# Performance work log

Hardware: AMD Instinct MI355X
Metric: run time of the kernel (lower is better)

The kernel has to match this reference:

```python
import jax, jax.numpy as jnp
import numpy as np

NEG_SLOPE = 0.2


def gat_conv(x, src, dst, W, a_src, a_dst, bias, heads, out_ch, concat, num_nodes):
    # x: [N, F_in]; W: [F_in, heads*out_ch]; a_src/a_dst: [heads, out_ch]
    h = (x @ W).reshape(num_nodes, heads, out_ch)                 # [N,H,C]
    alpha_s = jnp.sum(h * a_src[None], axis=-1)                   # [N,H]
    alpha_d = jnp.sum(h * a_dst[None], axis=-1)                   # [N,H]
    e = jax.nn.leaky_relu(alpha_s[src] + alpha_d[dst], NEG_SLOPE)  # [E,H]
    # numerically-stable segment softmax over incoming edges of each dst node
    e_max = jax.ops.segment_max(e, dst, num_segments=num_nodes)   # [N,H]
    e_exp = jnp.exp(e - e_max[dst])                               # [E,H]
    denom = jax.ops.segment_sum(e_exp, dst, num_segments=num_nodes)
    alpha = e_exp / (denom[dst] + 1e-16)                          # [E,H]
    msg = h[src] * alpha[:, :, None]                              # [E,H,C]
    out = jax.ops.segment_sum(msg, dst, num_segments=num_nodes)   # [N,H,C]
    if concat:
        out = out.reshape(num_nodes, heads * out_ch)
    else:
        out = out.mean(axis=1)
    return out + bias


def setup_inputs() -> dict:
    key = jax.random.key(0)
    ks = jax.random.split(key, 16)
    N, E = 100000, 1600000
    F_in, Hid, Out, Heads = 128, 64, 16, 1
    s = lambda k, shp, fan: jax.random.normal(k, shp, dtype=jnp.float32) * (1.0 / np.sqrt(fan))
    return {
        "x": jax.random.normal(ks[0], (N, F_in), dtype=jnp.float32),
        "edge_index": jax.random.randint(ks[1], (2, E), 0, N, dtype=jnp.int32),
        "W1": s(ks[2], (F_in, Heads * Hid), F_in),
        "a_src1": s(ks[3], (Heads, Hid), Hid),
        "a_dst1": s(ks[4], (Heads, Hid), Hid),
        "b1": jnp.zeros((Heads * Hid,), jnp.float32),
        "W2": s(ks[5], (Heads * Hid, Out), Heads * Hid),
        "a_src2": s(ks[6], (1, Out), Out),
        "a_dst2": s(ks[7], (1, Out), Out),
        "b2": jnp.zeros((Out,), jnp.float32),
        "lin1_W": s(ks[8], (Out, Hid), Out),
        "lin1_b": jnp.zeros((Hid,), jnp.float32),
        "lin2_W": s(ks[9], (Hid, Out), Hid),
        "lin2_b": jnp.zeros((Out,), jnp.float32),
    }


def reference(x, edge_index, W1, a_src1, a_dst1, b1, W2, a_src2, a_dst2, b2,
              lin1_W, lin1_b, lin2_W, lin2_b):
    N = x.shape[0]
    # PyG GATConv adds self-loops by default
    loop = jnp.arange(N, dtype=edge_index.dtype)
    src = jnp.concatenate([edge_index[0], loop])
    dst = jnp.concatenate([edge_index[1], loop])

    h = gat_conv(x, src, dst, W1, a_src1, a_dst1, b1,
                 heads=1, out_ch=64, concat=True, num_nodes=N)
    h = jax.nn.relu(h)
    h = gat_conv(h, src, dst, W2, a_src2, a_dst2, b2,
                 heads=1, out_ch=16, concat=False, num_nodes=N)
    h = jax.nn.relu(h @ lin1_W + lin1_b)
    h = h @ lin2_W + lin2_b
    return jax.nn.softmax(h, axis=-1)
```

## Files before the change

kernel.cpp:

```cpp
#include <hip/hip_runtime.h>

#define FIN 128
#define HID 64
#define OUTC 16
#define R1 16
#define BSH 8
#define MAXNB 512

__global__ __launch_bounds__(256) void k1_gemm1(
    const float* __restrict__ x, const float* __restrict__ W1,
    const float* __restrict__ a_src, const float* __restrict__ a_dst,
    float* __restrict__ h1, float* __restrict__ as1, float* __restrict__ ad1, int N)
{
    __shared__ float Wlds[FIN * HID];
    __shared__ float xlds[R1 * FIN];
    int tid = threadIdx.x;
    const float4* W4 = (const float4*)W1;
    float4* Wl4 = (float4*)Wlds;
    #pragma unroll
    for (int i = tid; i < FIN * HID / 4; i += 256) Wl4[i] = W4[i];
    int row0 = blockIdx.x * R1;
    const float4* x4 = (const float4*)(x + (size_t)row0 * FIN);
    float4* xl4 = (float4*)xlds;
    for (int i = tid; i < R1 * FIN / 4; i += 256) {
        int r = row0 + (i >> 5);
        xl4[i] = (r < N) ? x4[i] : make_float4(0.f, 0.f, 0.f, 0.f);
    }
    __syncthreads();
    int col = tid & 63;
    int wv  = tid >> 6;
    float acc[4] = {0.f, 0.f, 0.f, 0.f};
    #pragma unroll 4
    for (int k = 0; k < FIN; ++k) {
        float w = Wlds[k * HID + col];
        #pragma unroll
        for (int r = 0; r < 4; ++r)
            acc[r] += xlds[(wv * 4 + r) * FIN + k] * w;
    }
    #pragma unroll
    for (int r = 0; r < 4; ++r) {
        int row = row0 + wv * 4 + r;
        if (row < N) {
            h1[(size_t)row * HID + col] = acc[r];
            float vs = acc[r] * a_src[col];
            float vd = acc[r] * a_dst[col];
            for (int off = 32; off > 0; off >>= 1) {
                vs += __shfl_down(vs, off);
                vd += __shfl_down(vd, off);
            }
            if (col == 0) { as1[row] = vs; ad1[row] = vd; }
        }
    }
}

__global__ __launch_bounds__(256) void kp_cnt(
    const int* __restrict__ ei, int* __restrict__ bcnt, int E, int N)
{
    __shared__ int h[MAXNB];
    int tot = E + N;
    for (int i = threadIdx.x; i < MAXNB; i += 256) h[i] = 0;
    __syncthreads();
    int t0 = blockIdx.x * 4096;
    int n = min(4096, tot - t0);
    for (int i = threadIdx.x; i < n; i += 256) {
        int e = t0 + i;
        int d = (e < E) ? ei[E + e] : (e - E);
        atomicAdd(&h[d >> BSH], 1);
    }
    __syncthreads();
    int nb = (N + 255) >> BSH;
    for (int b = threadIdx.x; b < nb; b += 256)
        if (h[b]) atomicAdd(&bcnt[b], h[b]);
}

__global__ __launch_bounds__(512) void kp_scan(
    const int* __restrict__ bcnt, int* __restrict__ bstartE, int* __restrict__ bcur, int N)
{
    __shared__ int sA[512], sB[512];
    int nb = (N + 255) >> BSH;
    int tid = threadIdx.x;
    int c = (tid < nb) ? bcnt[tid] : 0;
    sA[tid] = c;
    __syncthreads();
    int* src = sA; int* dst = sB;
    for (int off = 1; off < 512; off <<= 1) {
        int v = src[tid];
        if (tid >= off) v += src[tid - off];
        dst[tid] = v;
        __syncthreads();
        int* t = src; src = dst; dst = t;
    }
    int incl = src[tid];
    int excl = incl - c;
    if (tid < nb) {
        bstartE[tid] = excl;
        bcur[tid] = excl;
        if (tid == nb - 1) bstartE[nb] = incl;
    }
}

__global__ __launch_bounds__(256) void kp_part(
    const int* __restrict__ ei, int* __restrict__ bcur, uint2* __restrict__ pairs,
    int E, int N)
{
    __shared__ int sL[4096], dL[4096];
    __shared__ int cnt[MAXNB], base[MAXNB], wcur[MAXNB];
    int tot = E + N;
    for (int i = threadIdx.x; i < MAXNB; i += 256) { cnt[i] = 0; wcur[i] = 0; }
    int t0 = blockIdx.x * 4096;
    int n = min(4096, tot - t0);
    for (int i = threadIdx.x; i < n; i += 256) {
        int e = t0 + i; int s, d;
        if (e < E) { s = ei[e]; d = ei[E + e]; } else { s = d = e - E; }
        sL[i] = s; dL[i] = d;
    }
    __syncthreads();
    for (int i = threadIdx.x; i < n; i += 256) atomicAdd(&cnt[dL[i] >> BSH], 1);
    __syncthreads();
    int nb = (N + 255) >> BSH;
    for (int b = threadIdx.x; b < nb; b += 256) {
        int c = cnt[b];
        if (c) base[b] = atomicAdd(&bcur[b], c);
    }
    __syncthreads();
    for (int i = threadIdx.x; i < n; i += 256) {
        int b = dL[i] >> BSH;
        int r = atomicAdd(&wcur[b], 1);
        pairs[base[b] + r] = make_uint2((unsigned)sL[i], (unsigned)dL[i]);
    }
}

__global__ __launch_bounds__(256) void kc_fine(
    const uint2* __restrict__ pairs, const int* __restrict__ bstartE,
    int* __restrict__ rowstart, int* __restrict__ counts, int* __restrict__ ssrc, int N)
{
    __shared__ int ncnt[256], nsA[256], nsB[256], nst[256];
    int blk = blockIdx.x, tid = threadIdx.x;
    int node0 = blk << BSH;
    int e0 = bstartE[blk], e1 = bstartE[blk + 1];
    ncnt[tid] = 0;
    __syncthreads();
    for (int i = e0 + tid; i < e1; i += 256)
        atomicAdd(&ncnt[pairs[i].y - node0], 1);
    __syncthreads();
    int c = ncnt[tid];
    nsA[tid] = c;
    __syncthreads();
    int* s = nsA; int* d = nsB;
    for (int off = 1; off < 256; off <<= 1) {
        int v = s[tid];
        if (tid >= off) v += s[tid - off];
        d[tid] = v;
        __syncthreads();
        int* t = s; s = d; d = t;
    }
    int excl = s[tid] - c;
    int node = node0 + tid;
    if (node < N) { rowstart[node] = e0 + excl; counts[node] = c; }
    __syncthreads();
    nst[tid] = excl;
    ncnt[tid] = 0;
    __syncthreads();
    for (int i = e0 + tid; i < e1; i += 256) {
        uint2 p = pairs[i];
        int dl = (int)p.y - node0;
        int r = atomicAdd(&ncnt[dl], 1);
        ssrc[e0 + nst[dl] + r] = (int)p.x;
    }
}

__global__ __launch_bounds__(256) void k_gat1(
    const int* __restrict__ rowstart, const int* __restrict__ counts,
    const int* __restrict__ ssrc,
    const float* __restrict__ as, const float* __restrict__ ad,
    const float* __restrict__ h, float* __restrict__ outp, int N)
{
    int wid = (blockIdx.x * 256 + threadIdx.x) >> 6;
    int lane = threadIdx.x & 63;
    if (wid >= N) return;
    int start = rowstart[wid];
    int deg   = counts[wid];
    float adv = ad[wid];
    float acc = 0.f, den = 0.f;
    int j = 0;
    for (; j + 4 <= deg; j += 4) {
        int s0 = ssrc[start + j + 0];
        int s1 = ssrc[start + j + 1];
        int s2 = ssrc[start + j + 2];
        int s3 = ssrc[start + j + 3];
        float a0 = as[s0], a1 = as[s1], a2 = as[s2], a3 = as[s3];
        float h0 = h[(size_t)s0 * HID + lane];
        float h1v = h[(size_t)s1 * HID + lane];
        float h2v = h[(size_t)s2 * HID + lane];
        float h3v = h[(size_t)s3 * HID + lane];
        float v0 = a0 + adv; v0 = (v0 > 0.f) ? v0 : 0.2f * v0; float w0 = __expf(v0);
        float v1 = a1 + adv; v1 = (v1 > 0.f) ? v1 : 0.2f * v1; float w1 = __expf(v1);
        float v2 = a2 + adv; v2 = (v2 > 0.f) ? v2 : 0.2f * v2; float w2 = __expf(v2);
        float v3 = a3 + adv; v3 = (v3 > 0.f) ? v3 : 0.2f * v3; float w3 = __expf(v3);
        den += (w0 + w1) + (w2 + w3);
        acc += w0 * h0;
        acc += w1 * h1v;
        acc += w2 * h2v;
        acc += w3 * h3v;
    }
    for (; j < deg; ++j) {
        int s = ssrc[start + j];
        float v = as[s] + adv;
        v = (v > 0.f) ? v : 0.2f * v;
        float w = __expf(v);
        den += w;
        acc += w * h[(size_t)s * HID + lane];
    }
    outp[(size_t)wid * HID + lane] = acc / (den + 1e-16f);
}

__global__ __launch_bounds__(256) void k4_gemm2(
    const float* __restrict__ out1, const float* __restrict__ b1,
    const float* __restrict__ W2, const float* __restrict__ a_src, const float* __restrict__ a_dst,
    float* __restrict__ h2, float* __restrict__ as2, float* __restrict__ ad2, int N)
{
    __shared__ float Wlds[HID * OUTC];
    __shared__ float rlds[16 * HID];
    int tid = threadIdx.x;
    for (int i = tid; i < HID * OUTC; i += 256) Wlds[i] = W2[i];
    int row0 = blockIdx.x * 16;
    for (int i = tid; i < 16 * HID; i += 256) {
        int r = row0 + (i >> 6);
        float v = (r < N) ? out1[(size_t)r * HID + (i & 63)] : 0.f;
        v += b1[i & 63];
        rlds[i] = fmaxf(v, 0.f);
    }
    __syncthreads();
    int col = tid & 15;
    int rl  = tid >> 4;
    int row = row0 + rl;
    float acc = 0.f;
    #pragma unroll 8
    for (int k = 0; k < HID; ++k)
        acc += rlds[rl * HID + k] * Wlds[k * OUTC + col];
    if (row < N) {
        h2[(size_t)row * OUTC + col] = acc;
        float vs = acc * a_src[col];
        float vd = acc * a_dst[col];
        for (int off = 8; off > 0; off >>= 1) {
            vs += __shfl_down(vs, off, 16);
            vd += __shfl_down(vd, off, 16);
        }
        if (col == 0) { as2[row] = vs; ad2[row] = vd; }
    }
}

__global__ __launch_bounds__(256) void k_gat2(
    const int* __restrict__ rowstart, const int* __restrict__ counts,
    const int* __restrict__ ssrc,
    const float* __restrict__ as, const float* __restrict__ ad,
    const float* __restrict__ h, float* __restrict__ outp, int N)
{
    int wid = (blockIdx.x * 256 + threadIdx.x) >> 6;
    int lane = threadIdx.x & 63;
    int c  = lane & 15;
    int eo = lane >> 4;
    if (wid >= N) return;
    int start = rowstart[wid];
    int deg   = counts[wid];
    float adv = ad[wid];
    float acc = 0.f, den = 0.f;
    int j = eo;
    for (; j + 4 < deg; j += 8) {
        int s0 = ssrc[start + j];
        int s1 = ssrc[start + j + 4];
        float a0 = as[s0], a1 = as[s1];
        float h0 = h[(size_t)s0 * OUTC + c];
        float h1v = h[(size_t)s1 * OUTC + c];
        float v0 = a0 + adv; v0 = (v0 > 0.f) ? v0 : 0.2f * v0; float w0 = __expf(v0);
        float v1 = a1 + adv; v1 = (v1 > 0.f) ? v1 : 0.2f * v1; float w1 = __expf(v1);
        den += w0 + w1;
        acc += w0 * h0;
        acc += w1 * h1v;
    }
    if (j < deg) {
        int s = ssrc[start + j];
        float v = as[s] + adv;
        v = (v > 0.f) ? v : 0.2f * v;
        float w = __expf(v);
        den += w;
        acc += w * h[(size_t)s * OUTC + c];
    }
    acc += __shfl_xor(acc, 16); den += __shfl_xor(den, 16);
    acc += __shfl_xor(acc, 32); den += __shfl_xor(den, 32);
    if (eo == 0) outp[(size_t)wid * OUTC + c] = acc / (den + 1e-16f);
}

__global__ __launch_bounds__(256) void k7_mlp(
    const float* __restrict__ out2, const float* __restrict__ b2,
    const float* __restrict__ lin1W, const float* __restrict__ lin1b,
    const float* __restrict__ lin2W, const float* __restrict__ lin2b,
    float* __restrict__ out, int N)
{
    __shared__ float W1l[OUTC * HID];
    __shared__ float W2l[HID * OUTC];
    __shared__ float b1l[HID], bb2[OUTC], b2l[OUTC];
    int tid = threadIdx.x;
    for (int i = tid; i < OUTC * HID; i += 256) { W1l[i] = lin1W[i]; W2l[i] = lin2W[i]; }
    if (tid < HID) b1l[tid] = lin1b[tid];
    if (tid < OUTC) { bb2[tid] = b2[tid]; b2l[tid] = lin2b[tid]; }
    __syncthreads();
    int n = blockIdx.x * 256 + tid;
    if (n >= N) return;

    float o[OUTC];
    const float4* o4 = (const float4*)(out2 + (size_t)n * OUTC);
    #pragma unroll
    for (int i = 0; i < 4; ++i) {
        float4 v = o4[i];
        o[4*i+0] = v.x + bb2[4*i+0];
        o[4*i+1] = v.y + bb2[4*i+1];
        o[4*i+2] = v.z + bb2[4*i+2];
        o[4*i+3] = v.w + bb2[4*i+3];
    }
    float u[OUTC];
    #pragma unroll
    for (int c = 0; c < OUTC; ++c) u[c] = b2l[c];
    for (int j = 0; j < HID; ++j) {
        float t = b1l[j];
        #pragma unroll
        for (int i = 0; i < OUTC; ++i) t += o[i] * W1l[i * HID + j];
        t = fmaxf(t, 0.f);
        #pragma unroll
        for (int c = 0; c < OUTC; ++c) u[c] += t * W2l[j * OUTC + c];
    }
    float m = u[0];
    #pragma unroll
    for (int c = 1; c < OUTC; ++c) m = fmaxf(m, u[c]);
    float sum = 0.f;
    #pragma unroll
    for (int c = 0; c < OUTC; ++c) { u[c] = __expf(u[c] - m); sum += u[c]; }
    float inv = 1.f / sum;
    float4* dst4 = (float4*)(out + (size_t)n * OUTC);
    #pragma unroll
    for (int i = 0; i < 4; ++i) {
        float4 v;
        v.x = u[4*i+0] * inv; v.y = u[4*i+1] * inv;
        v.z = u[4*i+2] * inv; v.w = u[4*i+3] * inv;
        dst4[i] = v;
    }
}

extern "C" void kernel_launch(void* const* d_in, const int* in_sizes, int n_in,
                              void* d_out, int out_size, void* d_ws, size_t ws_size,
                              hipStream_t stream)
{
    const float* x      = (const float*)d_in[0];
    const int*   ei     = (const int*)  d_in[1];
    const float* W1     = (const float*)d_in[2];
    const float* a_src1 = (const float*)d_in[3];
    const float* a_dst1 = (const float*)d_in[4];
    const float* b1     = (const float*)d_in[5];
    const float* W2     = (const float*)d_in[6];
    const float* a_src2 = (const float*)d_in[7];
    const float* a_dst2 = (const float*)d_in[8];
    const float* b2     = (const float*)d_in[9];
    const float* lin1W  = (const float*)d_in[10];
    const float* lin1b  = (const float*)d_in[11];
    const float* lin2W  = (const float*)d_in[12];
    const float* lin2b  = (const float*)d_in[13];
    float* out = (float*)d_out;

    int N = in_sizes[0] / FIN;
    int E = in_sizes[1] / 2;
    int tot = E + N;
    int nb = (N + 255) >> BSH;
    int ntile = (tot + 4095) / 4096;

    float* ws = (float*)d_ws;
    size_t off = 0;
    float* h1    = ws + off; off += (size_t)N * HID;
    float* out1  = ws + off; off += (size_t)N * HID;
    float* as1   = ws + off; off += N;
    float* ad1   = ws + off; off += N;
    float* h2    = ws + off; off += (size_t)N * OUTC;
    float* out2  = ws + off; off += (size_t)N * OUTC;
    float* as2   = ws + off; off += N;
    float* ad2   = ws + off; off += N;
    int* rowstart = (int*)(ws + off); off += N;
    int* counts   = (int*)(ws + off); off += N;
    int* ssrc     = (int*)(ws + off); off += tot;
    int* bcnt     = (int*)(ws + off); off += MAXNB;
    int* bstartE  = (int*)(ws + off); off += MAXNB + 1;
    int* bcur     = (int*)(ws + off); off += MAXNB;
    uint2* pairs  = (uint2*)out1;

    hipMemsetAsync(bcnt, 0, (size_t)nb * sizeof(int), stream);

    kp_cnt <<<ntile, 256, 0, stream>>>(ei, bcnt, E, N);
    kp_scan<<<1, 512, 0, stream>>>(bcnt, bstartE, bcur, N);
    kp_part<<<ntile, 256, 0, stream>>>(ei, bcur, pairs, E, N);
    kc_fine<<<nb, 256, 0, stream>>>(pairs, bstartE, rowstart, counts, ssrc, N);

    k1_gemm1<<<(N + R1 - 1) / R1, 256, 0, stream>>>(x, W1, a_src1, a_dst1, h1, as1, ad1, N);
    k_gat1  <<<(N + 3) / 4, 256, 0, stream>>>(rowstart, counts, ssrc, as1, ad1, h1, out1, N);

    k4_gemm2<<<(N + 15) / 16, 256, 0, stream>>>(out1, b1, W2, a_src2, a_dst2, h2, as2, ad2, N);
    k_gat2  <<<(N + 3) / 4, 256, 0, stream>>>(rowstart, counts, ssrc, as2, ad2, h2, out2, N);

    k7_mlp<<<(N + 255) / 256, 256, 0, stream>>>(out2, b2, lin1W, lin1b, lin2W, lin2b, out, N);
}
```

Measured before the change: 384.4 us.

## Precompute normalized edge attention weights in a separate pass; pack CSR build pairs

```diff
diff --git a/kernel.cpp b/kernel.cpp
--- a/kernel.cpp
+++ b/kernel.cpp
@@ -6,6 +6,11 @@
 #define R1 16
 #define BSH 8
 #define MAXNB 512
+
+__device__ __forceinline__ float lrelu_exp(float v) {
+    v = (v > 0.f) ? v : 0.2f * v;
+    return __expf(v);
+}
 
 __global__ __launch_bounds__(256) void k1_gemm1(
     const float* __restrict__ x, const float* __restrict__ W1,
@@ -30,12 +35,21 @@
     int col = tid & 63;
     int wv  = tid >> 6;
     float acc[4] = {0.f, 0.f, 0.f, 0.f};
+    const float4* xr0 = (const float4*)&xlds[(wv * 4 + 0) * FIN];
+    const float4* xr1 = (const float4*)&xlds[(wv * 4 + 1) * FIN];
+    const float4* xr2 = (const float4*)&xlds[(wv * 4 + 2) * FIN];
+    const float4* xr3 = (const float4*)&xlds[(wv * 4 + 3) * FIN];
     #pragma unroll 4
-    for (int k = 0; k < FIN; ++k) {
-        float w = Wlds[k * HID + col];
-        #pragma unroll
-        for (int r = 0; r < 4; ++r)
-            acc[r] += xlds[(wv * 4 + r) * FIN + k] * w;
+    for (int k4 = 0; k4 < FIN / 4; ++k4) {
+        float w0 = Wlds[(4 * k4 + 0) * HID + col];
+        float w1 = Wlds[(4 * k4 + 1) * HID + col];
+        float w2 = Wlds[(4 * k4 + 2) * HID + col];
+        float w3 = Wlds[(4 * k4 + 3) * HID + col];
+        float4 xv;
+        xv = xr0[k4]; acc[0] += xv.x * w0 + xv.y * w1 + xv.z * w2 + xv.w * w3;
+        xv = xr1[k4]; acc[1] += xv.x * w0 + xv.y * w1 + xv.z * w2 + xv.w * w3;
+        xv = xr2[k4]; acc[2] += xv.x * w0 + xv.y * w1 + xv.z * w2 + xv.w * w3;
+        xv = xr3[k4]; acc[3] += xv.x * w0 + xv.y * w1 + xv.z * w2 + xv.w * w3;
     }
     #pragma unroll
     for (int r = 0; r < 4; ++r) {
@@ -100,10 +114,11 @@
 }
 
 __global__ __launch_bounds__(256) void kp_part(
-    const int* __restrict__ ei, int* __restrict__ bcur, uint2* __restrict__ pairs,
+    const int* __restrict__ ei, int* __restrict__ bcur, unsigned* __restrict__ pairs,
     int E, int N)
 {
-    __shared__ int sL[4096], dL[4096];
+    __shared__ unsigned pk[4096];
+    __shared__ int bL[4096];
     __shared__ int cnt[MAXNB], base[MAXNB], wcur[MAXNB];
     int tot = E + N;
     for (int i = threadIdx.x; i < MAXNB; i += 256) { cnt[i] = 0; wcur[i] = 0; }
@@ -112,10 +127,11 @@
     for (int i = threadIdx.x; i < n; i += 256) {
         int e = t0 + i; int s, d;
         if (e < E) { s = ei[e]; d = ei[E + e]; } else { s = d = e - E; }
-        sL[i] = s; dL[i] = d;
-    }
-    __syncthreads();
-    for (int i = threadIdx.x; i < n; i += 256) atomicAdd(&cnt[dL[i] >> BSH], 1);
+        pk[i] = (unsigned)s | ((unsigned)(d & 255) << 24);
+        bL[i] = d >> BSH;
+    }
+    __syncthreads();
+    for (int i = threadIdx.x; i < n; i += 256) atomicAdd(&cnt[bL[i]], 1);
     __syncthreads();
     int nb = (N + 255) >> BSH;
     for (int b = threadIdx.x; b < nb; b += 256) {
@@ -124,14 +140,14 @@
     }
     __syncthreads();
     for (int i = threadIdx.x; i < n; i += 256) {
-        int b = dL[i] >> BSH;
+        int b = bL[i];
         int r = atomicAdd(&wcur[b], 1);
-        pairs[base[b] + r] = make_uint2((unsigned)sL[i], (unsigned)dL[i]);
+        pairs[base[b] + r] = pk[i];
     }
 }
 
 __global__ __launch_bounds__(256) void kc_fine(
-    const uint2* __restrict__ pairs, const int* __restrict__ bstartE,
+    const unsigned* __restrict__ pairs, const int* __restrict__ bstartE,
     int* __restrict__ rowstart, int* __restrict__ counts, int* __restrict__ ssrc, int N)
 {
     __shared__ int ncnt[256], nsA[256], nsB[256], nst[256];
@@ -141,7 +157,7 @@
     ncnt[tid] = 0;
     __syncthreads();
     for (int i = e0 + tid; i < e1; i += 256)
-        atomicAdd(&ncnt[pairs[i].y - node0], 1);
+        atomicAdd(&ncnt[pairs[i] >> 24], 1);
     __syncthreads();
     int c = ncnt[tid];
     nsA[tid] = c;
@@ -162,56 +178,104 @@
     ncnt[tid] = 0;
     __syncthreads();
     for (int i = e0 + tid; i < e1; i += 256) {
-        uint2 p = pairs[i];
-        int dl = (int)p.y - node0;
+        unsigned p = pairs[i];
+        int dl = (int)(p >> 24);
         int r = atomicAdd(&ncnt[dl], 1);
-        ssrc[e0 + nst[dl] + r] = (int)p.x;
-    }
-}
-
-__global__ __launch_bounds__(256) void k_gat1(
+        ssrc[e0 + nst[dl] + r] = (int)(p & 0xFFFFFFu);
+    }
+}
+
+__global__ __launch_bounds__(256) void k_wnorm(
     const int* __restrict__ rowstart, const int* __restrict__ counts,
-    const int* __restrict__ ssrc,
-    const float* __restrict__ as, const float* __restrict__ ad,
-    const float* __restrict__ h, float* __restrict__ outp, int N)
-{
-    int wid = (blockIdx.x * 256 + threadIdx.x) >> 6;
-    int lane = threadIdx.x & 63;
-    if (wid >= N) return;
-    int start = rowstart[wid];
-    int deg   = counts[wid];
-    float adv = ad[wid];
-    float acc = 0.f, den = 0.f;
+    const int* __restrict__ ssrc, const float* __restrict__ as, const float* __restrict__ ad,
+    float* __restrict__ alpha, int N)
+{
+    int n = blockIdx.x * 256 + threadIdx.x;
+    if (n >= N) return;
+    int start = rowstart[n];
+    int deg   = counts[n];
+    float adv = ad[n];
+    float den = 0.f;
     int j = 0;
     for (; j + 4 <= deg; j += 4) {
         int s0 = ssrc[start + j + 0];
         int s1 = ssrc[start + j + 1];
         int s2 = ssrc[start + j + 2];
         int s3 = ssrc[start + j + 3];
-        float a0 = as[s0], a1 = as[s1], a2 = as[s2], a3 = as[s3];
+        float w0 = lrelu_exp(as[s0] + adv);
+        float w1 = lrelu_exp(as[s1] + adv);
+        float w2 = lrelu_exp(as[s2] + adv);
+        float w3 = lrelu_exp(as[s3] + adv);
+        alpha[start + j + 0] = w0;
+        alpha[start + j + 1] = w1;
+        alpha[start + j + 2] = w2;
+        alpha[start + j + 3] = w3;
+        den += (w0 + w1) + (w2 + w3);
+    }
+    for (; j < deg; ++j) {
+        int s = ssrc[start + j];
+        float w = lrelu_exp(as[s] + adv);
+        alpha[start + j] = w;
+        den += w;
+    }
+    float inv = 1.f / (den + 1e-16f);
+    j = 0;
+    for (; j + 4 <= deg; j += 4) {
+        alpha[start + j + 0] *= inv;
+        alpha[start + j + 1] *= inv;
+        alpha[start + j + 2] *= inv;
+        alpha[start + j + 3] *= inv;
+    }
+    for (; j < deg; ++j) alpha[start + j] *= inv;
+}
+
+__global__ __launch_bounds__(256) void k_gat1(
+    const int* __restrict__ rowstart, const int* __restrict__ counts,
+    const int* __restrict__ ssrc, const float* __restrict__ alpha,
+    const float* __restrict__ h, float* __restrict__ outp, int N)
+{
+    int wid = (blockIdx.x * 256 + threadIdx.x) >> 6;
+    int lane = threadIdx.x & 63;
+    if (wid >= N) return;
+    int start = rowstart[wid];
+    int deg   = counts[wid];
+    float acc = 0.f;
+    int j = 0;
+    for (; j + 8 <= deg; j += 8) {
+        int s0 = ssrc[start + j + 0];
+        int s1 = ssrc[start + j + 1];
+        int s2 = ssrc[start + j + 2];
+        int s3 = ssrc[start + j + 3];
+        int s4 = ssrc[start + j + 4];
+        int s5 = ssrc[start + j + 5];
+        int s6 = ssrc[start + j + 6];
+        int s7 = ssrc[start + j + 7];
+        float a0 = alpha[start + j + 0];
+        float a1 = alpha[start + j + 1];
+        float a2 = alpha[start + j + 2];
+        float a3 = alpha[start + j + 3];
+        float a4 = alpha[start + j + 4];
+        float a5 = alpha[start + j + 5];
+        float a6 = alpha[start + j + 6];
+        float a7 = alpha[start + j + 7];
         float h0 = h[(size_t)s0 * HID + lane];
         float h1v = h[(size_t)s1 * HID + lane];
         float h2v = h[(size_t)s2 * HID + lane];
         float h3v = h[(size_t)s3 * HID + lane];
-        float v0 = a0 + adv; v0 = (v0 > 0.f) ? v0 : 0.2f * v0; float w0 = __expf(v0);
-        float v1 = a1 + adv; v1 = (v1 > 0.f) ? v1 : 0.2f * v1; float w1 = __expf(v1);
-        float v2 = a2 + adv; v2 = (v2 > 0.f) ? v2 : 0.2f * v2; float w2 = __expf(v2);
-        float v3 = a3 + adv; v3 = (v3 > 0.f) ? v3 : 0.2f * v3; float w3 = __expf(v3);
-        den += (w0 + w1) + (w2 + w3);
-        acc += w0 * h0;
-        acc += w1 * h1v;
-        acc += w2 * h2v;
-        acc += w3 * h3v;
+        float h4 = h[(size_t)s4 * HID + lane];
+        float h5 = h[(size_t)s5 * HID + lane];
+        float h6 = h[(size_t)s6 * HID + lane];
+        float h7 = h[(size_t)s7 * HID + lane];
+        acc += a0 * h0;  acc += a1 * h1v;
+        acc += a2 * h2v; acc += a3 * h3v;
+        acc += a4 * h4;  acc += a5 * h5;
+        acc += a6 * h6;  acc += a7 * h7;
     }
     for (; j < deg; ++j) {
         int s = ssrc[start + j];
-        float v = as[s] + adv;
-        v = (v > 0.f) ? v : 0.2f * v;
-        float w = __expf(v);
-        den += w;
-        acc += w * h[(size_t)s * HID + lane];
-    }
-    outp[(size_t)wid * HID + lane] = acc / (den + 1e-16f);
+        acc += alpha[start + j] * h[(size_t)s * HID + lane];
+    }
+    outp[(size_t)wid * HID + lane] = acc;
 }
 
 __global__ __launch_bounds__(256) void k4_gemm2(
@@ -252,8 +316,7 @@
 
 __global__ __launch_bounds__(256) void k_gat2(
     const int* __restrict__ rowstart, const int* __restrict__ counts,
-    const int* __restrict__ ssrc,
-    const float* __restrict__ as, const float* __restrict__ ad,
+    const int* __restrict__ ssrc, const float* __restrict__ alpha,
     const float* __restrict__ h, float* __restrict__ outp, int N)
 {
     int wid = (blockIdx.x * 256 + threadIdx.x) >> 6;
@@ -263,32 +326,25 @@
     if (wid >= N) return;
     int start = rowstart[wid];
     int deg   = counts[wid];
-    float adv = ad[wid];
-    float acc = 0.f, den = 0.f;
+    float acc = 0.f;
     int j = eo;
     for (; j + 4 < deg; j += 8) {
         int s0 = ssrc[start + j];
         int s1 = ssrc[start + j + 4];
-        float a0 = as[s0], a1 = as[s1];
+        float a0 = alpha[start + j];
+        float a1 = alpha[start + j + 4];
         float h0 = h[(size_t)s0 * OUTC + c];
         float h1v = h[(size_t)s1 * OUTC + c];
-        float v0 = a0 + adv; v0 = (v0 > 0.f) ? v0 : 0.2f * v0; float w0 = __expf(v0);
-        float v1 = a1 + adv; v1 = (v1 > 0.f) ? v1 : 0.2f * v1; float w1 = __expf(v1);
-        den += w0 + w1;
-        acc += w0 * h0;
-        acc += w1 * h1v;
+        acc += a0 * h0;
+        acc += a1 * h1v;
     }
     if (j < deg) {
         int s = ssrc[start + j];
-        float v = as[s] + adv;
-        v = (v > 0.f) ? v : 0.2f * v;
-        float w = __expf(v);
-        den += w;
-        acc += w * h[(size_t)s * OUTC + c];
-    }
-    acc += __shfl_xor(acc, 16); den += __shfl_xor(den, 16);
-    acc += __shfl_xor(acc, 32); den += __shfl_xor(den, 32);
-    if (eo == 0) outp[(size_t)wid * OUTC + c] = acc / (den + 1e-16f);
+        acc += alpha[start + j] * h[(size_t)s * OUTC + c];
+    }
+    acc += __shfl_xor(acc, 16);
+    acc += __shfl_xor(acc, 32);
+    if (eo == 0) outp[(size_t)wid * OUTC + c] = acc;
 }
 
 __global__ __launch_bounds__(256) void k7_mlp(
@@ -382,13 +438,14 @@
     float* out2  = ws + off; off += (size_t)N * OUTC;
     float* as2   = ws + off; off += N;
     float* ad2   = ws + off; off += N;
+    float* alpha = ws + off; off += tot;
     int* rowstart = (int*)(ws + off); off += N;
     int* counts   = (int*)(ws + off); off += N;
     int* ssrc     = (int*)(ws + off); off += tot;
     int* bcnt     = (int*)(ws + off); off += MAXNB;
     int* bstartE  = (int*)(ws + off); off += MAXNB + 1;
     int* bcur     = (int*)(ws + off); off += MAXNB;
-    uint2* pairs  = (uint2*)out1;
+    unsigned* pairs = (unsigned*)out1;
 
     hipMemsetAsync(bcnt, 0, (size_t)nb * sizeof(int), stream);
 
@@ -398,10 +455,12 @@
     kc_fine<<<nb, 256, 0, stream>>>(pairs, bstartE, rowstart, counts, ssrc, N);
 
     k1_gemm1<<<(N + R1 - 1) / R1, 256, 0, stream>>>(x, W1, a_src1, a_dst1, h1, as1, ad1, N);
-    k_gat1  <<<(N + 3) / 4, 256, 0, stream>>>(rowstart, counts, ssrc, as1, ad1, h1, out1, N);
+    k_wnorm <<<(N + 255) / 256, 256, 0, stream>>>(rowstart, counts, ssrc, as1, ad1, alpha, N);
+    k_gat1  <<<(N + 3) / 4, 256, 0, stream>>>(rowstart, counts, ssrc, alpha, h1, out1, N);
 
     k4_gemm2<<<(N + 15) / 16, 256, 0, stream>>>(out1, b1, W2, a_src2, a_dst2, h2, as2, ad2, N);
-    k_gat2  <<<(N + 3) / 4, 256, 0, stream>>>(rowstart, counts, ssrc, as2, ad2, h2, out2, N);
+    k_wnorm <<<(N + 255) / 256, 256, 0, stream>>>(rowstart, counts, ssrc, as2, ad2, alpha, N);
+    k_gat2  <<<(N + 3) / 4, 256, 0, stream>>>(rowstart, counts, ssrc, alpha, h2, out2, N);
 
     k7_mlp<<<(N + 255) / 256, 256, 0, stream>>>(out2, b2, lin1W, lin1b, lin2W, lin2b, out, N);
 }
```

New measurement: 425.6 us. 10.7% more time.
